# Optimization experiments

Measured on AMD Instinct MI355X. Metric: run time of the kernel, lower is better.

## Reference

```python
import jax, jax.numpy as jnp
import numpy as np

N = 16384
H = 256
C = 2


def setup_inputs() -> dict:
    key = jax.random.key(0)
    ks = jax.random.split(key, 9)
    s = lambda fan_in: 1.0 / np.sqrt(fan_in)
    return {
        "coordinates": jax.random.normal(ks[0], (N, C), dtype=jnp.float32) * 10.0,
        "W1": jax.random.normal(ks[1], (C, H), dtype=jnp.float32) * s(C),
        "b1": jnp.zeros((H,), dtype=jnp.float32),
        "W2": jax.random.normal(ks[2], (H, H), dtype=jnp.float32) * s(H),
        "b2": jnp.zeros((H,), dtype=jnp.float32),
        "Wd1": jax.random.normal(ks[3], (1, H // 2), dtype=jnp.float32) * s(1),
        "bd1": jnp.zeros((H // 2,), dtype=jnp.float32),
        "Wd2": jax.random.normal(ks[4], (H // 2, H), dtype=jnp.float32) * s(H // 2),
        "bd2": jnp.zeros((H,), dtype=jnp.float32),
        "k": 6,
    }


def reference(coordinates, W1, b1, W2, b2, Wd1, bd1, Wd2, bd2, k):
    x = coordinates.astype(jnp.float32)
    # coord MLP: Linear -> SiLU -> Linear
    coord_emb = jax.nn.silu(x @ W1 + b1) @ W2 + b2  # (N, H)

    # pairwise Euclidean distances (N, N), via ||a||^2 + ||b||^2 - 2ab
    sq = jnp.sum(x * x, axis=1)  # (N,)
    d2 = sq[:, None] + sq[None, :] - 2.0 * (x @ x.T)
    dist = jnp.sqrt(jnp.maximum(d2, 1e-12))  # safe sqrt; diag ~ 0

    # k+1 smallest distances per row (includes self at ~0), ascending
    kk = min(k + 1, dist.shape[1])
    neg_top, _ = jax.lax.top_k(-dist, kk)
    topk_dist = -neg_top  # ascending smallest
    mean_dist = jnp.mean(topk_dist[:, 1:], axis=1, keepdims=True)  # (N, 1)

    dist_emb = jax.nn.silu(mean_dist @ Wd1 + bd1) @ Wd2 + bd2  # (N, H)
    return coord_emb + dist_emb
```

## Files before the change

kernel.cpp:

```cpp
#include <hip/hip_runtime.h>
#include <float.h>
#include <math.h>

#define NPTS 16384
#define HDIM 256

#define KNB   256
#define KXMIN (-48.0f)
#define KW    0.375f
#define KINVW (1.0f / KW)

typedef __attribute__((ext_vector_type(8))) short bf16x8;
typedef __attribute__((ext_vector_type(4))) float f32x4;

__device__ __forceinline__ float silu_f(float z) {
    return z / (1.0f + __expf(-z));
}

__device__ __forceinline__ short f2bf(float f) {
    unsigned u = __float_as_uint(f);
    u = (u + 0x7FFFu + ((u >> 16) & 1u)) >> 16;
    return (short)u;
}

__device__ __forceinline__ float bcast_lane(float x, int l) {
    return __int_as_float(__builtin_amdgcn_readlane(__float_as_int(x), l));
}

__device__ __forceinline__ int binof(float x) {
    int b = (int)floorf((x - KXMIN) * KINVW);
    return b < 0 ? 0 : (b > KNB - 1 ? KNB - 1 : b);
}

#define INS7(a0,a1,a2,a3,a4,a5,a6,V)                \
    {   const float v_ = (V);                       \
        a6 = fmaxf(a5, fminf(a6, v_));              \
        a5 = fmaxf(a4, fminf(a5, v_));              \
        a4 = fmaxf(a3, fminf(a4, v_));              \
        a3 = fmaxf(a2, fminf(a3, v_));              \
        a2 = fmaxf(a1, fminf(a2, v_));              \
        a1 = fmaxf(a0, fminf(a1, v_));              \
        a0 = fminf(a0, v_);                         \
    }

__global__ __launch_bounds__(1024) void prep_kernel(
        const float* __restrict__ xyf,
        const float* __restrict__ W2, const float* __restrict__ Wd2,
        unsigned short* __restrict__ W2p, unsigned short* __restrict__ Wd2p,
        float2* __restrict__ sxy, unsigned* __restrict__ qidx,
        unsigned* __restrict__ off) {
    const int tid = threadIdx.x;

    if (blockIdx.x < 12) {
        const int slot = blockIdx.x * 1024 + tid;
        const float* src;
        unsigned short* dst;
        int s;
        if (slot < 8192) { src = W2;  dst = W2p;  s = slot; }
        else             { src = Wd2; dst = Wd2p; s = slot - 8192; }
        const int t   = s >> 10;
        const int rem = s & 1023;
        const int ct  = rem >> 6;
        const int l   = rem & 63;
        const int k0  = t * 32 + 8 * (l >> 4);
        const int c   = ct * 16 + (l & 15);
        bf16x8 v;
        #pragma unroll
        for (int i = 0; i < 8; ++i)
            v[i] = f2bf(src[(size_t)(k0 + i) * HDIM + c]);
        ((bf16x8*)dst)[s] = v;
        return;
    }

    __shared__ unsigned h[KNB];
    __shared__ unsigned sc[KNB];
    __shared__ unsigned cur[KNB];
    if (tid < KNB) h[tid] = 0u;
    __syncthreads();
    for (int i = tid; i < NPTS; i += 1024)
        atomicAdd(&h[binof(xyf[2 * i])], 1u);
    __syncthreads();
    unsigned own = 0u;
    if (tid < KNB) { own = h[tid]; sc[tid] = own; }
    __syncthreads();
    for (int s = 1; s < KNB; s <<= 1) {
        unsigned v = 0u;
        if (tid < KNB && tid >= s) v = sc[tid - s];
        __syncthreads();
        if (tid < KNB) sc[tid] += v;
        __syncthreads();
    }
    if (tid < KNB) {
        const unsigned excl = sc[tid] - own;
        off[tid] = excl;
        cur[tid] = excl;
    }
    if (tid == 0) off[KNB] = (unsigned)NPTS;
    __syncthreads();
    for (int i = tid; i < NPTS; i += 1024) {
        const float2 p = ((const float2*)xyf)[i];
        const unsigned pos = atomicAdd(&cur[binof(p.x)], 1u);
        sxy[pos]  = p;
        qidx[pos] = (unsigned)i;
    }
}

__global__ __launch_bounds__(512, 8) void knn_search(const float2* __restrict__ sxy,
                                                     const unsigned* __restrict__ qidx,
                                                     const unsigned* __restrict__ off,
                                                     float* __restrict__ md) {
    const int lane = threadIdx.x & 63;
    const int wv   = threadIdx.x >> 6;
    const int qpos = blockIdx.x * 8 + wv;
    const float2 q = sxy[qpos];

    float s0 = FLT_MAX, s1 = FLT_MAX, s2 = FLT_MAX, s3 = FLT_MAX,
          s4 = FLT_MAX, s5 = FLT_MAX, s6 = FLT_MAX;

    const int b0 = binof(q.x);
    const int lb = b0 > 0 ? b0 - 1 : 0;
    const int rb = b0 < KNB - 1 ? b0 + 1 : KNB - 1;

    {
        const unsigned o = off[lb], e = off[rb + 1];
        for (unsigned u = o + (unsigned)lane; u < e; u += 64u) {
            const float2 p = sxy[u];
            const float dx = q.x - p.x, dy = q.y - p.y;
            const float d2 = fmaf(dx, dx, dy * dy);
            if (d2 < s6) INS7(s0, s1, s2, s3, s4, s5, s6, d2)
        }
    }

    #pragma unroll
    for (int m = 1; m < 64; m <<= 1) {
        const float o0 = __shfl_xor(s0, m);
        const float o1 = __shfl_xor(s1, m);
        const float o2 = __shfl_xor(s2, m);
        const float o3 = __shfl_xor(s3, m);
        const float o4 = __shfl_xor(s4, m);
        const float o5 = __shfl_xor(s5, m);
        const float o6 = __shfl_xor(s6, m);
        const float n0 = fminf(s0, o0);
        const float n1 = fminf(fminf(s1, o1), fmaxf(s0, o0));
        const float n2 = fminf(fminf(s2, o2),
                               fminf(fmaxf(s0, o1), fmaxf(s1, o0)));
        const float n3 = fminf(fminf(s3, o3),
                               fminf(fmaxf(s0, o2),
                                     fminf(fmaxf(s1, o1), fmaxf(s2, o0))));
        const float n4 = fminf(fminf(s4, o4),
                               fminf(fminf(fmaxf(s0, o3), fmaxf(s1, o2)),
                                     fminf(fmaxf(s2, o1), fmaxf(s3, o0))));
        const float n5 = fminf(fminf(s5, o5),
                               fminf(fminf(fmaxf(s0, o4), fmaxf(s1, o3)),
                                     fminf(fmaxf(s2, o2),
                                           fminf(fmaxf(s3, o1), fmaxf(s4, o0)))));
        const float n6 = fminf(fminf(s6, o6),
                               fminf(fminf(fmaxf(s0, o5), fmaxf(s1, o4)),
                                     fminf(fmaxf(s2, o3),
                                           fminf(fmaxf(s3, o2),
                                                 fminf(fmaxf(s4, o1),
                                                       fmaxf(s5, o0))))));
        s0 = n0; s1 = n1; s2 = n2; s3 = n3; s4 = n4; s5 = n5; s6 = n6;
    }

    int l = lb - 1, r = rb + 1;
    while (l >= 0 || r < KNB) {
        float bl = FLT_MAX, br = FLT_MAX;
        if (l >= 0) {
            const float d = fmaxf(q.x - (KXMIN + (float)(l + 1) * KW), 0.0f);
            bl = d * d;
        }
        if (r < KNB) {
            const float d = fmaxf((KXMIN + (float)r * KW) - q.x, 0.0f);
            br = d * d;
        }
        if (fminf(bl, br) > s6) break;
        const int b = (bl <= br) ? l : r;
        const unsigned o = off[b], e = off[b + 1];
        for (unsigned u = o; u < e; u += 64u) {
            const unsigned idx = u + (unsigned)lane;
            float d2 = FLT_MAX;
            if (idx < e) {
                const float2 p = sxy[idx];
                const float dx = q.x - p.x, dy = q.y - p.y;
                d2 = fmaf(dx, dx, dy * dy);
            }
            unsigned long long m = __ballot(d2 < s6);
            while (m) {
                const int L   = __ffsll(m) - 1;
                const float v = bcast_lane(d2, L);
                INS7(s0, s1, s2, s3, s4, s5, s6, v)
                if (lane == L) d2 = FLT_MAX;
                m = __ballot(d2 < s6);
            }
        }
        if (bl <= br) --l; else ++r;
    }

    if (lane == 0) {
        const float sum = sqrtf(fmaxf(s1, 1e-12f)) + sqrtf(fmaxf(s2, 1e-12f)) +
                          sqrtf(fmaxf(s3, 1e-12f)) + sqrtf(fmaxf(s4, 1e-12f)) +
                          sqrtf(fmaxf(s5, 1e-12f)) + sqrtf(fmaxf(s6, 1e-12f));
        md[qidx[qpos]] = sum * (1.0f / 6.0f);
    }
}

#define GEN_A(T)                                                              \
    {                                                                         \
        const int kb = (T) * 32 + klane;                                      \
        const float4 p0 = *(const float4*)(W1 + kb);                          \
        const float4 p1 = *(const float4*)(W1 + kb + 4);                      \
        const float4 r0_ = *(const float4*)(W1 + HDIM + kb);                  \
        const float4 r1_ = *(const float4*)(W1 + HDIM + kb + 4);              \
        const float4 c0_ = *(const float4*)(b1 + kb);                         \
        const float4 c1_ = *(const float4*)(b1 + kb + 4);                     \
        const float pw[8] = {p0.x,p0.y,p0.z,p0.w,p1.x,p1.y,p1.z,p1.w};        \
        const float rw[8] = {r0_.x,r0_.y,r0_.z,r0_.w,r1_.x,r1_.y,r1_.z,r1_.w};\
        const float cw[8] = {c0_.x,c0_.y,c0_.z,c0_.w,c1_.x,c1_.y,c1_.z,c1_.w};\
        _Pragma("unroll")                                                     \
        for (int i = 0; i < 8; ++i)                                           \
            a[i] = f2bf(silu_f(fmaf(q.x, pw[i], fmaf(q.y, rw[i], cw[i]))));   \
    }

#define GEN_G(T)                                                              \
    {                                                                         \
        const int kb = (T) * 32 + klane;                                      \
        const float4 p0 = *(const float4*)(Wd1 + kb);                         \
        const float4 p1 = *(const float4*)(Wd1 + kb + 4);                     \
        const float4 c0_ = *(const float4*)(bd1 + kb);                        \
        const float4 c1_ = *(const float4*)(bd1 + kb + 4);                    \
        const float pw[8] = {p0.x,p0.y,p0.z,p0.w,p1.x,p1.y,p1.z,p1.w};        \
        const float cw[8] = {c0_.x,c0_.y,c0_.z,c0_.w,c1_.x,c1_.y,c1_.z,c1_.w};\
        _Pragma("unroll")                                                     \
        for (int i = 0; i < 8; ++i)                                           \
            a[i] = f2bf(silu_f(fmaf(mdr, pw[i], cw[i])));                     \
    }

#define MFMA8(BUF)                                                            \
    _Pragma("unroll")                                                         \
    for (int j = 0; j < 8; ++j)                                               \
        acc[j] = __builtin_amdgcn_mfma_f32_16x16x32_bf16(a, BUF[j], acc[j], 0, 0, 0);

#define LOADB(BUF, ARR, T)                                                    \
    _Pragma("unroll")                                                         \
    for (int j = 0; j < 8; ++j)                                               \
        BUF[j] = ARR[((T) * 16 + ch * 8 + j) * 64 + lane];

__global__ __launch_bounds__(256, 2) void mlp_kernel(
        const float* __restrict__ xyf,
        const float* __restrict__ W1,  const float* __restrict__ b1,
        const float* __restrict__ b2,
        const float* __restrict__ Wd1, const float* __restrict__ bd1,
        const float* __restrict__ bd2,
        const unsigned short* __restrict__ W2p,
        const unsigned short* __restrict__ Wd2p,
        const float* __restrict__ md,  float* __restrict__ out) {
    const int tid  = threadIdx.x;
    const int lane = tid & 63;
    const int w    = tid >> 6;
    const int r0   = blockIdx.x * 32 + (w >> 1) * 16;
    const int ch   = w & 1;
    const int row  = r0 + (lane & 15);
    const float2 q = ((const float2*)xyf)[row];
    const float mdr = md[row];
    const int klane = 8 * (lane >> 4);

    f32x4 acc[8];
    #pragma unroll
    for (int j = 0; j < 8; ++j) {
        acc[j][0] = 0.0f; acc[j][1] = 0.0f; acc[j][2] = 0.0f; acc[j][3] = 0.0f;
    }

    const bf16x8* B1 = (const bf16x8*)W2p;
    const bf16x8* B2 = (const bf16x8*)Wd2p;
    bf16x8 bA[8], bB[8];
    bf16x8 a;

    LOADB(bA, B1, 0)

    #pragma unroll
    for (int tt = 0; tt < 4; ++tt) {
        {   const int t = 2 * tt;
            GEN_A(t)
            LOADB(bB, B1, t + 1)
            MFMA8(bA)
        }
        {   const int t = 2 * tt + 1;
            GEN_A(t)
            if (t + 1 < 8) { LOADB(bA, B1, t + 1) }
            else           { LOADB(bA, B2, 0)     }
            MFMA8(bB)
        }
    }

    #pragma unroll
    for (int uu = 0; uu < 2; ++uu) {
        {   const int t = 2 * uu;
            GEN_G(t)
            LOADB(bB, B2, t + 1)
            MFMA8(bA)
        }
        {   const int t = 2 * uu + 1;
            GEN_G(t)
            if (t + 1 < 4) { LOADB(bA, B2, t + 1) }
            MFMA8(bB)
        }
    }

    const int cb = ch * 128;
    const int rr = r0 + 4 * (lane >> 4);
    #pragma unroll
    for (int j = 0; j < 8; ++j) {
        const int c = cb + j * 16 + (lane & 15);
        const float add = b2[c] + bd2[c];
        out[(size_t)(rr + 0) * HDIM + c] = acc[j][0] + add;
        out[(size_t)(rr + 1) * HDIM + c] = acc[j][1] + add;
        out[(size_t)(rr + 2) * HDIM + c] = acc[j][2] + add;
        out[(size_t)(rr + 3) * HDIM + c] = acc[j][3] + add;
    }
}

extern "C" void kernel_launch(void* const* d_in, const int* in_sizes, int n_in,
                              void* d_out, int out_size, void* d_ws, size_t ws_size,
                              hipStream_t stream) {
    const float* xy  = (const float*)d_in[0];
    const float* W1  = (const float*)d_in[1];
    const float* b1  = (const float*)d_in[2];
    const float* W2  = (const float*)d_in[3];
    const float* b2  = (const float*)d_in[4];
    const float* Wd1 = (const float*)d_in[5];
    const float* bd1 = (const float*)d_in[6];
    const float* Wd2 = (const float*)d_in[7];
    const float* bd2 = (const float*)d_in[8];
    float* out = (float*)d_out;

    char* ws = (char*)d_ws;
    float*          md   = (float*)ws;
    unsigned short* W2p  = (unsigned short*)(ws + 65536);
    unsigned short* Wd2p = (unsigned short*)(ws + 196608);
    unsigned*       off  = (unsigned*)(ws + 262144);
    float2*         sxy  = (float2*)(ws + 263424);
    unsigned*       qidx = (unsigned*)(ws + 394496);

    prep_kernel<<<13, 1024, 0, stream>>>(xy, W2, Wd2, W2p, Wd2p, sxy, qidx, off);
    knn_search<<<NPTS / 8, 512, 0, stream>>>(sxy, qidx, off, md);
    mlp_kernel<<<NPTS / 32, 256, 0, stream>>>(xy, W1, b1, b2, Wd1, bd1, bd2,
                                              W2p, Wd2p, md, out);
}
```

Before: 168.5 us.

## Use per-wave histograms and nearest-nonempty bin tables for KNN expansion

The prep kernel now keeps one bin histogram per wavefront instead of a single shared one. This spreads the shared-memory atomic contention during counting and scattering. Alongside the prefix sum it builds nearest-nonempty-bin tables, which the KNN search uses to jump over empty bins while expanding outward. The KNN launch also drops to 256-thread blocks of 4 queries each. In exchange the prep kernel does extra scan work and uses more shared memory, and the search does one extra global load per step.

```diff
diff --git a/kernel.cpp b/kernel.cpp
--- a/kernel.cpp
+++ b/kernel.cpp
@@ -48,7 +48,7 @@
         const float* __restrict__ W2, const float* __restrict__ Wd2,
         unsigned short* __restrict__ W2p, unsigned short* __restrict__ Wd2p,
         float2* __restrict__ sxy, unsigned* __restrict__ qidx,
-        unsigned* __restrict__ off) {
+        unsigned* __restrict__ off, int* __restrict__ lne, int* __restrict__ rne) {
     const int tid = threadIdx.x;
 
     if (blockIdx.x < 12) {
@@ -72,46 +72,74 @@
         return;
     }
 
-    __shared__ unsigned h[KNB];
+    __shared__ unsigned cnt[16][KNB];
+    __shared__ unsigned tot[KNB];
     __shared__ unsigned sc[KNB];
-    __shared__ unsigned cur[KNB];
-    if (tid < KNB) h[tid] = 0u;
+    __shared__ int      li[KNB];
+    __shared__ int      ri[KNB];
+    const int w = tid >> 6;
+
+    for (int i = tid; i < 16 * KNB; i += 1024) ((unsigned*)cnt)[i] = 0u;
     __syncthreads();
     for (int i = tid; i < NPTS; i += 1024)
-        atomicAdd(&h[binof(xyf[2 * i])], 1u);
+        atomicAdd(&cnt[w][binof(xyf[2 * i])], 1u);
     __syncthreads();
-    unsigned own = 0u;
-    if (tid < KNB) { own = h[tid]; sc[tid] = own; }
+
+    if (tid < KNB) {
+        unsigned run = 0u;
+        #pragma unroll
+        for (int ww = 0; ww < 16; ++ww) {
+            const unsigned t_ = cnt[ww][tid];
+            cnt[ww][tid] = run;
+            run += t_;
+        }
+        tot[tid] = run;
+        sc[tid]  = run;
+        li[tid]  = run ? tid : -1;
+        ri[tid]  = run ? tid : KNB;
+    }
     __syncthreads();
     for (int s = 1; s < KNB; s <<= 1) {
-        unsigned v = 0u;
-        if (tid < KNB && tid >= s) v = sc[tid - s];
+        unsigned v = 0u; int lv = -1, rv = KNB;
+        if (tid < KNB) {
+            if (tid >= s)       { v  = sc[tid - s]; lv = li[tid - s]; }
+            if (tid + s < KNB)  { rv = ri[tid + s]; }
+        }
         __syncthreads();
-        if (tid < KNB) sc[tid] += v;
+        if (tid < KNB) {
+            sc[tid] += v;
+            li[tid] = li[tid] > lv ? li[tid] : lv;
+            ri[tid] = ri[tid] < rv ? ri[tid] : rv;
+        }
         __syncthreads();
     }
     if (tid < KNB) {
-        const unsigned excl = sc[tid] - own;
+        const unsigned excl = sc[tid] - tot[tid];
         off[tid] = excl;
-        cur[tid] = excl;
+        lne[tid] = li[tid];
+        rne[tid] = ri[tid];
+        #pragma unroll
+        for (int ww = 0; ww < 16; ++ww) cnt[ww][tid] += excl;
     }
     if (tid == 0) off[KNB] = (unsigned)NPTS;
     __syncthreads();
     for (int i = tid; i < NPTS; i += 1024) {
         const float2 p = ((const float2*)xyf)[i];
-        const unsigned pos = atomicAdd(&cur[binof(p.x)], 1u);
+        const unsigned pos = atomicAdd(&cnt[w][binof(p.x)], 1u);
         sxy[pos]  = p;
         qidx[pos] = (unsigned)i;
     }
 }
 
-__global__ __launch_bounds__(512, 8) void knn_search(const float2* __restrict__ sxy,
+__global__ __launch_bounds__(256, 8) void knn_search(const float2* __restrict__ sxy,
                                                      const unsigned* __restrict__ qidx,
                                                      const unsigned* __restrict__ off,
+                                                     const int* __restrict__ lne,
+                                                     const int* __restrict__ rne,
                                                      float* __restrict__ md) {
     const int lane = threadIdx.x & 63;
     const int wv   = threadIdx.x >> 6;
-    const int qpos = blockIdx.x * 8 + wv;
+    const int qpos = blockIdx.x * 4 + wv;
     const float2 q = sxy[qpos];
 
     float s0 = FLT_MAX, s1 = FLT_MAX, s2 = FLT_MAX, s3 = FLT_MAX,
@@ -164,7 +192,10 @@
     }
 
     int l = lb - 1, r = rb + 1;
-    while (l >= 0 || r < KNB) {
+    while (true) {
+        l = (l >= 0) ? lne[l] : -1;
+        r = (r < KNB) ? rne[r] : KNB;
+        if (l < 0 && r >= KNB) break;
         float bl = FLT_MAX, br = FLT_MAX;
         if (l >= 0) {
             const float d = fmaxf(q.x - (KXMIN + (float)(l + 1) * KW), 0.0f);
@@ -341,9 +372,12 @@
     unsigned*       off  = (unsigned*)(ws + 262144);
     float2*         sxy  = (float2*)(ws + 263424);
     unsigned*       qidx = (unsigned*)(ws + 394496);
-
-    prep_kernel<<<13, 1024, 0, stream>>>(xy, W2, Wd2, W2p, Wd2p, sxy, qidx, off);
-    knn_search<<<NPTS / 8, 512, 0, stream>>>(sxy, qidx, off, md);
+    int*            lne  = (int*)(ws + 460032);
+    int*            rne  = (int*)(ws + 461056);
+
+    prep_kernel<<<13, 1024, 0, stream>>>(xy, W2, Wd2, W2p, Wd2p, sxy, qidx,
+                                         off, lne, rne);
+    knn_search<<<NPTS / 4, 256, 0, stream>>>(sxy, qidx, off, lne, rne, md);
     mlp_kernel<<<NPTS / 32, 256, 0, stream>>>(xy, W1, b1, b2, Wd1, bd1, bd2,
                                               W2p, Wd2p, md, out);
 }
```

Result: slower. 174.6 us (+3.6%).

## Parallelise histogram and scatter prep across multiple blocks, split knn launch

Applied to the files above, without the earlier changes.

Replaces the single-block histogram/scan/scatter prep with a two-kernel scheme. Twelve blocks build partial per-bin histograms, then twelve blocks each derive their own prefix offsets and scatter their slice of points. This targets the serial single-block bottleneck in building the binned point layout. The knn search is also issued as two half-sized launches, which adds an extra kernel launch.

```diff
diff --git a/kernel.cpp b/kernel.cpp
--- a/kernel.cpp
+++ b/kernel.cpp
@@ -9,6 +9,7 @@
 #define KXMIN (-48.0f)
 #define KW    0.375f
 #define KINVW (1.0f / KW)
+#define NHB   12
 
 typedef __attribute__((ext_vector_type(8))) short bf16x8;
 typedef __attribute__((ext_vector_type(4))) float f32x4;
@@ -43,16 +44,15 @@
         a0 = fminf(a0, v_);                         \
     }
 
-__global__ __launch_bounds__(1024) void prep_kernel(
+__global__ __launch_bounds__(256) void prepA_kernel(
         const float* __restrict__ xyf,
         const float* __restrict__ W2, const float* __restrict__ Wd2,
         unsigned short* __restrict__ W2p, unsigned short* __restrict__ Wd2p,
-        float2* __restrict__ sxy, unsigned* __restrict__ qidx,
-        unsigned* __restrict__ off) {
+        unsigned* __restrict__ histp) {
     const int tid = threadIdx.x;
 
-    if (blockIdx.x < 12) {
-        const int slot = blockIdx.x * 1024 + tid;
+    if (blockIdx.x < 48) {
+        const int slot = blockIdx.x * 256 + tid;
         const float* src;
         unsigned short* dst;
         int s;
@@ -72,32 +72,49 @@
         return;
     }
 
-    __shared__ unsigned h[KNB];
+    __shared__ unsigned lh[KNB];
+    const int h = blockIdx.x - 48;
+    lh[tid] = 0u;
+    __syncthreads();
+    for (int i = h * 256 + tid; i < NPTS; i += NHB * 256)
+        atomicAdd(&lh[binof(xyf[2 * i])], 1u);
+    __syncthreads();
+    histp[h * KNB + tid] = lh[tid];
+}
+
+__global__ __launch_bounds__(256) void prepB_kernel(
+        const float* __restrict__ xyf,
+        const unsigned* __restrict__ histp,
+        unsigned* __restrict__ off,
+        float2* __restrict__ sxy, unsigned* __restrict__ qidx) {
     __shared__ unsigned sc[KNB];
     __shared__ unsigned cur[KNB];
-    if (tid < KNB) h[tid] = 0u;
-    __syncthreads();
-    for (int i = tid; i < NPTS; i += 1024)
-        atomicAdd(&h[binof(xyf[2 * i])], 1u);
-    __syncthreads();
-    unsigned own = 0u;
-    if (tid < KNB) { own = h[tid]; sc[tid] = own; }
+    const int tid = threadIdx.x;
+    const int myb = blockIdx.x;
+
+    unsigned tot = 0u, pre = 0u;
+    #pragma unroll
+    for (int b = 0; b < NHB; ++b) {
+        const unsigned v = histp[b * KNB + tid];
+        if (b < myb) pre += v;
+        tot += v;
+    }
+    sc[tid] = tot;
     __syncthreads();
     for (int s = 1; s < KNB; s <<= 1) {
-        unsigned v = 0u;
-        if (tid < KNB && tid >= s) v = sc[tid - s];
+        const unsigned v = (tid >= s) ? sc[tid - s] : 0u;
         __syncthreads();
-        if (tid < KNB) sc[tid] += v;
+        sc[tid] += v;
         __syncthreads();
     }
-    if (tid < KNB) {
-        const unsigned excl = sc[tid] - own;
+    const unsigned excl = sc[tid] - tot;
+    cur[tid] = excl + pre;
+    if (myb == 0) {
         off[tid] = excl;
-        cur[tid] = excl;
-    }
-    if (tid == 0) off[KNB] = (unsigned)NPTS;
+        if (tid == 0) off[KNB] = (unsigned)NPTS;
+    }
     __syncthreads();
-    for (int i = tid; i < NPTS; i += 1024) {
+    for (int i = myb * 256 + tid; i < NPTS; i += NHB * 256) {
         const float2 p = ((const float2*)xyf)[i];
         const unsigned pos = atomicAdd(&cur[binof(p.x)], 1u);
         sxy[pos]  = p;
@@ -108,10 +125,11 @@
 __global__ __launch_bounds__(512, 8) void knn_search(const float2* __restrict__ sxy,
                                                      const unsigned* __restrict__ qidx,
                                                      const unsigned* __restrict__ off,
-                                                     float* __restrict__ md) {
+                                                     float* __restrict__ md,
+                                                     int qbase) {
     const int lane = threadIdx.x & 63;
     const int wv   = threadIdx.x >> 6;
-    const int qpos = blockIdx.x * 8 + wv;
+    const int qpos = qbase + blockIdx.x * 8 + wv;
     const float2 q = sxy[qpos];
 
     float s0 = FLT_MAX, s1 = FLT_MAX, s2 = FLT_MAX, s3 = FLT_MAX,
@@ -335,15 +353,18 @@
     float* out = (float*)d_out;
 
     char* ws = (char*)d_ws;
-    float*          md   = (float*)ws;
-    unsigned short* W2p  = (unsigned short*)(ws + 65536);
-    unsigned short* Wd2p = (unsigned short*)(ws + 196608);
-    unsigned*       off  = (unsigned*)(ws + 262144);
-    float2*         sxy  = (float2*)(ws + 263424);
-    unsigned*       qidx = (unsigned*)(ws + 394496);
-
-    prep_kernel<<<13, 1024, 0, stream>>>(xy, W2, Wd2, W2p, Wd2p, sxy, qidx, off);
-    knn_search<<<NPTS / 8, 512, 0, stream>>>(sxy, qidx, off, md);
+    float*          md    = (float*)ws;
+    unsigned short* W2p   = (unsigned short*)(ws + 65536);
+    unsigned short* Wd2p  = (unsigned short*)(ws + 196608);
+    unsigned*       off   = (unsigned*)(ws + 262144);
+    float2*         sxy   = (float2*)(ws + 263424);
+    unsigned*       qidx  = (unsigned*)(ws + 394496);
+    unsigned*       histp = (unsigned*)(ws + 460032);
+
+    prepA_kernel<<<60, 256, 0, stream>>>(xy, W2, Wd2, W2p, Wd2p, histp);
+    prepB_kernel<<<NHB, 256, 0, stream>>>(xy, histp, off, sxy, qidx);
+    knn_search<<<NPTS / 16, 512, 0, stream>>>(sxy, qidx, off, md, 0);
+    knn_search<<<NPTS / 16, 512, 0, stream>>>(sxy, qidx, off, md, NPTS / 2);
     mlp_kernel<<<NPTS / 32, 256, 0, stream>>>(xy, W1, b1, b2, Wd1, bd1, bd2,
                                               W2p, Wd2p, md, out);
 }
```

Result: slower. 189.2 us (+12.3%).
